# Optimization experiments

Measured on AMD Instinct MI355X. Metric: run time of the kernel, lower is better.

## Reference

```python
import jax, jax.numpy as jnp
import numpy as np

N = 4096
CIN = 128
COUT = 128
J = 2
DENSITY = 0.01  # ~40 nonzeros per Laplacian row


def _mask(k):
    m = (jax.random.uniform(k, (N, N)) < DENSITY).astype(jnp.float32)
    # Laplacians have nonzero diagonals; also guarantees no empty softmax rows
    return jnp.maximum(m, jnp.eye(N, dtype=jnp.float32))


def setup_inputs() -> dict:
    key = jax.random.key(0)
    ks = jax.random.split(key, 9)
    x = jax.random.normal(ks[0], (N, CIN), dtype=jnp.float32)
    Lup = _mask(ks[1])
    Ldown = _mask(ks[2])
    P = jax.random.normal(ks[3], (N, N), dtype=jnp.float32) / np.float32(np.sqrt(N))
    weight_irr = jax.random.normal(ks[4], (J, CIN, COUT), dtype=jnp.float32) * 0.05
    weight_sol = jax.random.normal(ks[5], (J, CIN, COUT), dtype=jnp.float32) * 0.05
    weight_har = jax.random.normal(ks[6], (CIN, COUT), dtype=jnp.float32) * 0.05
    att_irr = jax.random.normal(ks[7], (2 * J * COUT, 1), dtype=jnp.float32) * 0.05
    att_sol = jax.random.normal(ks[8], (2 * J * COUT, 1), dtype=jnp.float32) * 0.05
    return {"x": x, "Lup": Lup, "Ldown": Ldown, "P": P,
            "weight_irr": weight_irr, "weight_sol": weight_sol,
            "weight_har": weight_har, "att_irr": att_irr, "att_sol": att_sol}


def _masked_row_softmax(e, mask):
    # torch.sparse.softmax over the mask's nonzero pattern, dim=1, then to_dense
    on = mask > 0
    z = jnp.where(on, e, -jnp.inf)
    m = jnp.max(z, axis=1, keepdims=True)
    m = jnp.where(jnp.isfinite(m), m, 0.0)  # guard fully-masked rows
    p = jnp.exp(z - m)                      # exp(-inf)=0 off-pattern
    s = jnp.sum(p, axis=1, keepdims=True)
    s = jnp.where(s == 0, 1.0, s)
    return jnp.where(on, p / s, 0.0)


def _branch(x, weight, att, mask):
    j, cout = weight.shape[0], weight.shape[2]
    att_slice = j * cout
    h = jnp.einsum('ni,jio->jno', x, weight)         # [J, N, Cout]
    hf = h.reshape(-1, att_slice)                    # [N, J*Cout] (row-major, as torch)
    src = hf @ att[:att_slice]                       # [N, 1]
    dst = hf @ att[att_slice:]                       # [N, 1]
    e = jax.nn.leaky_relu(src + dst.T)               # [N, N], slope 0.01 (torch default)
    alpha = _masked_row_softmax(e, mask)             # [N, N]
    powers = [alpha]
    for _ in range(j - 1):
        powers.append(powers[-1] @ alpha)            # iterative matrix powers
    alpha_exp = jnp.stack(powers)                    # [J, N, N]
    # torch.sum with no dim: full reduction to a SCALAR (faithful to source)
    return jnp.sum(jnp.einsum('jnm,jmo->jno', alpha_exp, h))


def reference(x, Lup, Ldown, P, weight_irr, weight_sol, weight_har, att_irr, att_sol):
    z_irr = _branch(x, weight_irr, att_irr, Ldown)   # scalar
    z_sol = _branch(x, weight_sol, att_sol, Lup)     # scalar
    z_har = (P @ x) @ weight_har                     # [N, Cout]
    return z_irr + z_sol + z_har
```

## Files before the change

### kernel.cpp

```cpp
#include <hip/hip_runtime.h>

typedef __attribute__((ext_vector_type(8))) short short8b;
typedef __attribute__((ext_vector_type(4))) float f32x4;

#define NEG_SENTINEL (-1e30f)

constexpr int C_OFF    = 0;
constexpr int C2_OFF   = 8192;
constexpr int SC_OFF   = 16384;
constexpr int FLAG_I   = 16390;
constexpr int ZERO_N   = 16448;
constexpr int V_OFF    = 16448;
constexpr int NP_OFF   = 19008;
constexpr int SRC_OFF  = 100928;
constexpr int RM_OFF   = 117312;
constexpr int RS_OFF   = 125504;
constexpr int NNZ_OFF  = 133696;
constexpr int CCI_OFF  = 141888;
constexpr int XBT_OFF  = 666176;
constexpr int TP_OFF   = 928320;

__device__ __forceinline__ unsigned short f2bf(float f) {
  unsigned int u = __float_as_uint(f);
  u += 0x7FFFu + ((u >> 16) & 1u);
  return (unsigned short)(u >> 16);
}
__device__ __forceinline__ float bf2f(unsigned short b) {
  return __uint_as_float(((unsigned int)b) << 16);
}
__device__ __forceinline__ float scrub(float v) {
  unsigned int u = __float_as_uint(v);
  return ((u & 0x7F800000u) == 0x7F800000u) ? 0.f : v;
}

__global__ __launch_bounds__(128) void k_vvec(const void* __restrict__ xin,
                                              const void* __restrict__ w_irr,
                                              const void* __restrict__ w_sol,
                                              const void* __restrict__ att_irr,
                                              const void* __restrict__ att_sol,
                                              int* __restrict__ flagp,
                                              float* __restrict__ vvec) {
  __shared__ int sdet[128];
  int t = threadIdx.x;
  unsigned int ef = (((const unsigned int*)xin)[t] >> 7) & 0xFFu;
  sdet[t] = (ef >= 100u && ef <= 150u) ? 1 : 0;
  __syncthreads();
  for (int d = 64; d > 0; d >>= 1) { if (t < d) sdet[t] += sdet[t + d]; __syncthreads(); }
  int f = (sdet[0] >= 96) ? 1 : 0;
  if (blockIdx.x == 0 && t == 0) *flagp = f;
  int bx = blockIdx.x;
  int b = bx / 10, rem = bx % 10, j = rem / 5, tt = rem % 5;
  const void* Wv = (b == 0 ? w_irr : w_sol);
  const void* Av = (b == 0 ? att_irr : att_sol);
  int i = t;
  float s = 0.f;
  if (f) {
    const unsigned short* Wr = (const unsigned short*)Wv + (size_t)j * 16384 + (size_t)i * 128;
    const unsigned short* Ar = (const unsigned short*)Av + tt * 128;
    for (int o = 0; o < 128; o += 8) {
      uint4 wq = *(const uint4*)(Wr + o);
      unsigned int ww[4] = {wq.x, wq.y, wq.z, wq.w};
      float cf[8];
      if (tt < 4) {
        uint4 aq = *(const uint4*)(Ar + o);
        unsigned int aa[4] = {aq.x, aq.y, aq.z, aq.w};
#pragma unroll
        for (int u = 0; u < 4; ++u) {
          cf[2 * u] = bf2f((unsigned short)(aa[u] & 0xFFFFu));
          cf[2 * u + 1] = bf2f((unsigned short)(aa[u] >> 16));
        }
      } else {
#pragma unroll
        for (int e = 0; e < 8; ++e) cf[e] = 1.0f;
      }
#pragma unroll
      for (int u = 0; u < 4; ++u) {
        s += bf2f((unsigned short)(ww[u] & 0xFFFFu)) * cf[2 * u];
        s += bf2f((unsigned short)(ww[u] >> 16)) * cf[2 * u + 1];
      }
    }
  } else {
    const float* Wr = (const float*)Wv + (size_t)j * 16384 + (size_t)i * 128;
    const float* Ar = (const float*)Av + tt * 128;
    for (int o = 0; o < 128; o += 4) {
      float4 wq = *(const float4*)(Wr + o);
      float4 aq = {1.f, 1.f, 1.f, 1.f};
      if (tt < 4) aq = *(const float4*)(Ar + o);
      s += wq.x * aq.x + wq.y * aq.y + wq.z * aq.z + wq.w * aq.w;
    }
  }
  vvec[bx * 128 + i] = s;
}

__global__ __launch_bounds__(256) void k_prep(const void* __restrict__ xin,
                                              const int* __restrict__ flag,
                                              const float* __restrict__ vvec,
                                              unsigned short* __restrict__ xbT,
                                              float* __restrict__ np,
                                              float* __restrict__ srcdst) {
  __shared__ __align__(16) float ldsx[64 * 130];
  __shared__ __align__(16) float ldsv[2560];
  __shared__ float ldsp[4 * 1280];
  __shared__ float npl[1280];
  int f = *flag;
  int t = threadIdx.x, nb = blockIdx.x * 64;
  for (int q = 0; q < 16; ++q) {
    int idx = q * 256 + t;
    int row = idx >> 6, cp = idx & 63;
    float vx, vy;
    if (f) {
      unsigned int u = ((const unsigned int*)xin)[(size_t)(nb + row) * 64 + cp];
      vx = bf2f((unsigned short)(u & 0xFFFFu));
      vy = bf2f((unsigned short)(u >> 16));
    } else {
      float2 v = ((const float2*)xin)[(size_t)(nb + row) * 64 + cp];
      vx = v.x; vy = v.y;
    }
    ldsx[row * 130 + cp * 2] = vx;
    ldsx[row * 130 + cp * 2 + 1] = vy;
  }
  for (int q = 0; q < 10; ++q) { int idx = q * 256 + t; ldsv[idx] = vvec[idx]; }
  __syncthreads();
  for (int q = 0; q < 32; ++q) {
    int idx = q * 256 + t;
    int c = idx >> 6, n = idx & 63;
    xbT[(size_t)c * 4096 + nb + n] = f2bf(ldsx[n * 130 + c]);
  }
  int row = t & 63, qq = t >> 6, i0 = qq * 32;
  float acc[20];
#pragma unroll
  for (int k = 0; k < 20; ++k) acc[k] = 0.f;
  for (int i = i0; i < i0 + 32; i += 2) {
    float2 xv = *(const float2*)&ldsx[row * 130 + i];
#pragma unroll
    for (int k = 0; k < 20; ++k) {
      float2 vk = *(const float2*)&ldsv[k * 128 + i];
      acc[k] += xv.x * vk.x + xv.y * vk.y;
    }
  }
#pragma unroll
  for (int k = 0; k < 20; ++k) ldsp[qq * 1280 + row * 20 + k] = acc[k];
  __syncthreads();
  for (int rep = 0; rep < 5; ++rep) {
    int idx = rep * 256 + t;
    int k = idx >> 6, rr = idx & 63;
    float s = ldsp[rr * 20 + k] + ldsp[1280 + rr * 20 + k] +
              ldsp[2560 + rr * 20 + k] + ldsp[3840 + rr * 20 + k];
    npl[k * 64 + rr] = s;
    np[(size_t)k * 4096 + nb + rr] = s;
  }
  __syncthreads();
  {
    int b = t >> 7, j = (t >> 6) & 1, kind = (t >> 5) & 1, q = t & 31;
    int bl = q * 2;
    int r = j * 2048 + (nb >> 1) + q;
    int kidx = b * 10 + j * 5 + kind * 2;
    float val = npl[kidx * 64 + bl] + npl[(kidx + 1) * 64 + bl + 1];
    srcdst[b * 8192 + kind * 4096 + r] = val;
  }
}

__device__ __forceinline__ int col_of(int f, int l, int bit) {
  if (f) return ((bit >> 3) * 512) + l * 8 + (bit & 7);
  return ((bit >> 5) * 2048) + (((bit >> 2) & 7) * 256) + l * 4 + (bit & 3);
}

__global__ __launch_bounds__(256) void k_scan(const void* __restrict__ Ldown,
                                              const void* __restrict__ Lup,
                                              float* __restrict__ ws) {
  int b = blockIdx.y, t = threadIdx.x;
  int wid = t >> 6, l = t & 63;
  int r = blockIdx.x * 4 + wid;
  int f = ((const int*)ws)[FLAG_I];
  unsigned short* cci = (unsigned short*)(ws + CCI_OFF) + (size_t)(b * 4096 + r) * 128;
  unsigned long long hm = 0ULL;
  if (f) {
    const uint4* rp = (const uint4*)((const unsigned short*)(b ? Lup : Ldown) +
                                     (size_t)r * 4096) + l;
    uint4 cs[8];
#pragma unroll
    for (int it = 0; it < 8; ++it) cs[it] = rp[it * 64];
#pragma unroll
    for (int it = 0; it < 8; ++it) {
      unsigned int wv[4] = {cs[it].x, cs[it].y, cs[it].z, cs[it].w};
#pragma unroll
      for (int u = 0; u < 4; ++u) {
        hm |= ((unsigned long long)((wv[u] & 0xFFFFu) != 0u)) << (it * 8 + u * 2);
        hm |= ((unsigned long long)((wv[u] >> 16) != 0u)) << (it * 8 + u * 2 + 1);
      }
    }
  } else {
    const uint4* rp = (const uint4*)((const float*)(b ? Lup : Ldown) +
                                     (size_t)r * 4096) + l;
#pragma unroll
    for (int p = 0; p < 2; ++p) {
      uint4 cs[8];
#pragma unroll
      for (int it = 0; it < 8; ++it) cs[it] = rp[(p * 8 + it) * 64];
#pragma unroll
      for (int it = 0; it < 8; ++it) {
        unsigned int wv[4] = {cs[it].x, cs[it].y, cs[it].z, cs[it].w};
#pragma unroll
        for (int u = 0; u < 4; ++u)
          hm |= ((unsigned long long)(wv[u] != 0u)) << (p * 32 + it * 4 + u);
      }
    }
  }
  int cnt = __popcll(hm);
  int pre = cnt;
  for (int d = 1; d < 64; d <<= 1) {
    int o = __shfl_up(pre, d);
    if (l >= d) pre += o;
  }
  int base = pre - cnt;
  int nz = __shfl(pre, 63);
  if (l == 0) ((int*)ws)[NNZ_OFF + b * 4096 + r] = min(nz, 128);
  const float* srcp = ws + SRC_OFF + b * 8192;
  const float* dstp = srcp + 4096;
  float srcr = srcp[r];
  float mx = NEG_SENTINEL, sm = 0.f;
  unsigned long long mm = hm;
  while (mm) {
    int bit = __builtin_ctzll(mm); mm &= mm - 1;
    int m = col_of(f, l, bit);
    float e = srcr + dstp[m];
    e = (e >= 0.f) ? e : 0.01f * e;
    if (e > mx) { sm = sm * __expf(mx - e) + 1.f; mx = e; }
    else        { sm += __expf(e - mx); }
  }
  for (int d = 1; d < 64; d <<= 1) {
    float om = __shfl_xor(mx, d);
    float os = __shfl_xor(sm, d);
    float M = fmaxf(mx, om);
    sm = sm * __expf(mx - M) + os * __expf(om - M);
    mx = M;
  }
  if (l == 0) {
    ws[RM_OFF + b * 4096 + r] = mx;
    ws[RS_OFF + b * 4096 + r] = sm;
  }
  float inv = 1.0f / sm;
  int slot = base;
  mm = hm;
  while (mm) {
    int bit = __builtin_ctzll(mm); mm &= mm - 1;
    int m = col_of(f, l, bit);
    if (slot < 128) cci[slot] = (unsigned short)m;
    ++slot;
    float e = srcr + dstp[m];
    e = (e >= 0.f) ? e : 0.01f * e;
    atomicAdd(&ws[C_OFF + b * 4096 + m], __expf(e - mx) * inv);
  }
}

__device__ __forceinline__ float alpha_of(const float* ws, int b, int r, int m) {
  const float* srcp = ws + SRC_OFF + b * 8192;
  float e = srcp[r] + srcp[4096 + m];
  e = (e >= 0.f) ? e : 0.01f * e;
  return __expf(e - ws[RM_OFF + b * 4096 + r]) / ws[RS_OFF + b * 4096 + r];
}

__global__ __launch_bounds__(256) void k_c2(float* __restrict__ ws) {
  int b = blockIdx.y;
  int s = blockIdx.x * 256 + threadIdx.x;
  int r = s >> 7, k = s & 127;
  int nz = ((const int*)ws)[NNZ_OFF + b * 4096 + r];
  if (k < nz) {
    int m = ((const unsigned short*)(ws + CCI_OFF))[(size_t)(b * 4096 + r) * 128 + k];
    atomicAdd(&ws[C2_OFF + b * 4096 + m], ws[C_OFF + b * 4096 + r] * alpha_of(ws, b, r, m));
  }
}

__global__ __launch_bounds__(256) void k_scalar(float* __restrict__ ws) {
  int b = blockIdx.x, t = threadIdx.x;
  const float* cb  = ws + C_OFF  + b * 4096;
  const float* c2b = ws + C2_OFF + b * 4096;
  const float* hr0 = ws + NP_OFF + (b * 10 + 4) * 4096;
  const float* hr1 = ws + NP_OFF + (b * 10 + 9) * 4096;
  double acc = 0.0;
  for (int m = t; m < 4096; m += 256)
    acc += (double)scrub(cb[m]) * (double)scrub(hr0[m]) +
           (double)scrub(c2b[m]) * (double)scrub(hr1[m]);
  __shared__ double sd[256];
  sd[t] = acc;
  __syncthreads();
  for (int s = 128; s > 0; s >>= 1) { if (t < s) sd[t] += sd[t + s]; __syncthreads(); }
  if (t == 0) atomicAdd(&ws[SC_OFF], (float)sd[0]);
}

__global__ __launch_bounds__(256) void k_gemm1(const void* __restrict__ P,
                                               const unsigned short* __restrict__ xbT,
                                               const int* __restrict__ flag,
                                               float* __restrict__ TP) {
  __shared__ __align__(16) unsigned short a_lds[64 * 40];
  __shared__ __align__(16) unsigned short b_lds[128 * 40];
  int f = *flag;
  const int mt = blockIdx.x & 63, ks = blockIdx.x >> 6;
  const int mb = mt * 64;
  const int t = threadIdx.x;
  const int w = t >> 6, l = t & 63, quad = l >> 4, lr = l & 15;
  f32x4 acc[8] = {};
  const int arow = t >> 2, akq = (t & 3) << 3;
  const int bn = t >> 1, bh = (t & 1) << 4;
  const int k0 = ks * 512;
  uint4 aU, bU0, bU1;
#define LOADT(IT)                                                              \
  {                                                                            \
    const int kb = k0 + (IT) * 32;                                             \
    if (f) {                                                                   \
      aU = *(const uint4*)((const unsigned short*)P +                          \
                           (size_t)(mb + arow) * 4096 + kb + akq);             \
    } else {                                                                   \
      const float* pa = (const float*)P + (size_t)(mb + arow) * 4096 + kb + akq; \
      float4 f0 = *(const float4*)pa;                                          \
      float4 f1 = *(const float4*)(pa + 4);                                    \
      unsigned short u[8] = {f2bf(f0.x), f2bf(f0.y), f2bf(f0.z), f2bf(f0.w),   \
                             f2bf(f1.x), f2bf(f1.y), f2bf(f1.z), f2bf(f1.w)};  \
      aU = *(const uint4*)u;                                                   \
    }                                                                          \
    const unsigned short* src = xbT + (size_t)bn * 4096 + kb + bh;             \
    bU0 = *(const uint4*)src;                                                  \
    bU1 = *(const uint4*)(src + 8);                                            \
  }
  LOADT(0);
  for (int it = 0; it < 16; ++it) {
    *(uint4*)&a_lds[arow * 40 + akq] = aU;
    *(uint4*)&b_lds[bn * 40 + bh] = bU0;
    *(uint4*)&b_lds[bn * 40 + bh + 8] = bU1;
    __syncthreads();
    if (it < 15) LOADT(it + 1);
    short8b af = *(short8b*)&a_lds[(w * 16 + lr) * 40 + quad * 8];
#pragma unroll
    for (int nt = 0; nt < 8; ++nt) {
      short8b bf = *(short8b*)&b_lds[(nt * 16 + lr) * 40 + quad * 8];
      acc[nt] = __builtin_amdgcn_mfma_f32_16x16x32_bf16(af, bf, acc[nt], 0, 0, 0);
    }
    if (it < 15) __syncthreads();
  }
#undef LOADT
  float* Tp = TP + (size_t)ks * 524288;
#pragma unroll
  for (int nt = 0; nt < 8; ++nt)
#pragma unroll
    for (int rr = 0; rr < 4; ++rr) {
      int row = mb + w * 16 + quad * 4 + rr;
      int col = nt * 16 + lr;
      Tp[(size_t)row * 128 + col] = acc[nt][rr];
    }
}

__global__ __launch_bounds__(256) void k_gemm2(const float* __restrict__ TP,
                                               const void* __restrict__ W,
                                               const float* __restrict__ ws,
                                               void* __restrict__ outv) {
  __shared__ float tl[16 * 128];
  int f = ((const int*)ws)[FLAG_I];
  int t = threadIdx.x;
  int rb = blockIdx.x * 16;
  for (int q = 0; q < 2; ++q) {
    int vi = q * 256 + t;
    size_t base = (size_t)rb * 128 + (size_t)vi * 4;
    float4 s = {0.f, 0.f, 0.f, 0.f};
#pragma unroll
    for (int p = 0; p < 8; ++p) {
      float4 v = *(const float4*)&TP[(size_t)p * 524288 + base];
      s.x += v.x; s.y += v.y; s.z += v.z; s.w += v.w;
    }
    *(float4*)&tl[vi * 4] = s;
  }
  __syncthreads();
  int col = t & 127, rg = t >> 7;
  int r0 = rg * 8;
  float acc[8] = {};
  for (int k = 0; k < 128; k += 4) {
    float w0, w1, w2, w3;
    if (f) {
      const unsigned short* W16 = (const unsigned short*)W;
      w0 = bf2f(W16[(k + 0) * 128 + col]); w1 = bf2f(W16[(k + 1) * 128 + col]);
      w2 = bf2f(W16[(k + 2) * 128 + col]); w3 = bf2f(W16[(k + 3) * 128 + col]);
    } else {
      const float* W32 = (const float*)W;
      w0 = W32[(k + 0) * 128 + col]; w1 = W32[(k + 1) * 128 + col];
      w2 = W32[(k + 2) * 128 + col]; w3 = W32[(k + 3) * 128 + col];
    }
#pragma unroll
    for (int rr = 0; rr < 8; ++rr) {
      float4 tv = *(const float4*)&tl[(r0 + rr) * 128 + k];
      acc[rr] += tv.x * w0 + tv.y * w1 + tv.z * w2 + tv.w * w3;
    }
  }
  float s = scrub(ws[SC_OFF]);
#pragma unroll
  for (int rr = 0; rr < 8; ++rr) {
    size_t oi = (size_t)(rb + r0 + rr) * 128 + col;
    float v = s + acc[rr];
    if (f) ((unsigned short*)outv)[oi] = f2bf(v);
    else   ((float*)outv)[oi] = v;
  }
}

extern "C" void kernel_launch(void* const* d_in, const int* in_sizes, int n_in,
                              void* d_out, int out_size, void* d_ws, size_t ws_size,
                              hipStream_t stream) {
  const void* x       = d_in[0];
  const void* Lup     = d_in[1];
  const void* Ldown   = d_in[2];
  const void* P       = d_in[3];
  const void* w_irr   = d_in[4];
  const void* w_sol   = d_in[5];
  const void* w_har   = d_in[6];
  const void* att_irr = d_in[7];
  const void* att_sol = d_in[8];
  float* ws = (float*)d_ws;

  hipMemsetAsync(d_ws, 0, (size_t)ZERO_N * sizeof(float), stream);
  k_vvec  <<<20, 128, 0, stream>>>(x, w_irr, w_sol, att_irr, att_sol,
                                   (int*)ws + FLAG_I, ws + V_OFF);
  k_prep  <<<64, 256, 0, stream>>>(x, (int*)ws + FLAG_I, ws + V_OFF,
                                   (unsigned short*)(ws + XBT_OFF), ws + NP_OFF,
                                   ws + SRC_OFF);
  k_gemm1 <<<512, 256, 0, stream>>>(P, (const unsigned short*)(ws + XBT_OFF),
                                    (int*)ws + FLAG_I, ws + TP_OFF);
  k_scan  <<<dim3(1024, 2), 256, 0, stream>>>(Ldown, Lup, ws);
  k_c2    <<<dim3(2048, 2), 256, 0, stream>>>(ws);
  k_scalar<<<2, 256, 0, stream>>>(ws);
  k_gemm2 <<<256, 256, 0, stream>>>(ws + TP_OFF, w_har, ws, d_out);
}
```

Baseline: 308.1 us.

## Split softmax into a separate kernel with cached alpha values, and reorder launches

The mask-scan kernel now only compacts column indices. A new k_smax kernel computes the row softmax from the compacted indices with one wave per row and two values per lane, stores the alpha values, and scatters them into C. k_c2 reads the stored alpha values instead of recomputing exp and divide per nonzero, and its grid is halved to one wave per row. The sparse kernels now launch before gemm1 because the alpha buffer aliases the TP region that gemm1 writes. This adds a kernel launch and an extra buffer round trip in exchange for less divergent serial work in the scan.

```diff
diff --git a/kernel.cpp b/kernel.cpp
--- a/kernel.cpp
+++ b/kernel.cpp
@@ -19,6 +19,7 @@
 constexpr int CCI_OFF  = 141888;
 constexpr int XBT_OFF  = 666176;
 constexpr int TP_OFF   = 928320;
+constexpr int AV_OFF   = 928320;
 
 __device__ __forceinline__ unsigned short f2bf(float f) {
   unsigned int u = __float_as_uint(f);
@@ -215,60 +216,71 @@
   int base = pre - cnt;
   int nz = __shfl(pre, 63);
   if (l == 0) ((int*)ws)[NNZ_OFF + b * 4096 + r] = min(nz, 128);
-  const float* srcp = ws + SRC_OFF + b * 8192;
-  const float* dstp = srcp + 4096;
-  float srcr = srcp[r];
-  float mx = NEG_SENTINEL, sm = 0.f;
+  int slot = base;
   unsigned long long mm = hm;
-  while (mm) {
-    int bit = __builtin_ctzll(mm); mm &= mm - 1;
-    int m = col_of(f, l, bit);
-    float e = srcr + dstp[m];
-    e = (e >= 0.f) ? e : 0.01f * e;
-    if (e > mx) { sm = sm * __expf(mx - e) + 1.f; mx = e; }
-    else        { sm += __expf(e - mx); }
-  }
-  for (int d = 1; d < 64; d <<= 1) {
-    float om = __shfl_xor(mx, d);
-    float os = __shfl_xor(sm, d);
-    float M = fmaxf(mx, om);
-    sm = sm * __expf(mx - M) + os * __expf(om - M);
-    mx = M;
-  }
-  if (l == 0) {
-    ws[RM_OFF + b * 4096 + r] = mx;
-    ws[RS_OFF + b * 4096 + r] = sm;
-  }
-  float inv = 1.0f / sm;
-  int slot = base;
-  mm = hm;
   while (mm) {
     int bit = __builtin_ctzll(mm); mm &= mm - 1;
     int m = col_of(f, l, bit);
     if (slot < 128) cci[slot] = (unsigned short)m;
     ++slot;
-    float e = srcr + dstp[m];
-    e = (e >= 0.f) ? e : 0.01f * e;
-    atomicAdd(&ws[C_OFF + b * 4096 + m], __expf(e - mx) * inv);
-  }
-}
-
-__device__ __forceinline__ float alpha_of(const float* ws, int b, int r, int m) {
+  }
+}
+
+__global__ __launch_bounds__(256) void k_smax(float* __restrict__ ws) {
+  int b = blockIdx.y, t = threadIdx.x;
+  int wid = t >> 6, l = t & 63;
+  int r = blockIdx.x * 4 + wid;
+  int nz = ((const int*)ws)[NNZ_OFF + b * 4096 + r];
+  const unsigned short* cci =
+      (const unsigned short*)(ws + CCI_OFF) + (size_t)(b * 4096 + r) * 128;
   const float* srcp = ws + SRC_OFF + b * 8192;
-  float e = srcp[r] + srcp[4096 + m];
-  e = (e >= 0.f) ? e : 0.01f * e;
-  return __expf(e - ws[RM_OFF + b * 4096 + r]) / ws[RS_OFF + b * 4096 + r];
+  const float* dstp = srcp + 4096;
+  float srcr = srcp[r];
+  int m0 = 0, m1 = 0;
+  float e0 = NEG_SENTINEL, e1 = NEG_SENTINEL;
+  if (l < nz) {
+    m0 = cci[l];
+    float e = srcr + dstp[m0];
+    e0 = (e >= 0.f) ? e : 0.01f * e;
+  }
+  if (l + 64 < nz) {
+    m1 = cci[l + 64];
+    float e = srcr + dstp[m1];
+    e1 = (e >= 0.f) ? e : 0.01f * e;
+  }
+  float mx = fmaxf(e0, e1);
+  for (int d = 1; d < 64; d <<= 1) mx = fmaxf(mx, __shfl_xor(mx, d));
+  float p0 = (l < nz) ? __expf(e0 - mx) : 0.f;
+  float p1 = (l + 64 < nz) ? __expf(e1 - mx) : 0.f;
+  float sm = p0 + p1;
+  for (int d = 1; d < 64; d <<= 1) sm += __shfl_xor(sm, d);
+  float inv = 1.0f / sm;
+  float* av = ws + AV_OFF + (size_t)(b * 4096 + r) * 128;
+  if (l < nz) {
+    float a = p0 * inv;
+    av[l] = a;
+    atomicAdd(&ws[C_OFF + b * 4096 + m0], a);
+  }
+  if (l + 64 < nz) {
+    float a = p1 * inv;
+    av[l + 64] = a;
+    atomicAdd(&ws[C2_OFF - C2_OFF + C_OFF + b * 4096 + m1], a);
+  }
 }
 
 __global__ __launch_bounds__(256) void k_c2(float* __restrict__ ws) {
-  int b = blockIdx.y;
-  int s = blockIdx.x * 256 + threadIdx.x;
-  int r = s >> 7, k = s & 127;
+  int b = blockIdx.y, t = threadIdx.x;
+  int wid = t >> 6, l = t & 63;
+  int r = blockIdx.x * 4 + wid;
   int nz = ((const int*)ws)[NNZ_OFF + b * 4096 + r];
-  if (k < nz) {
-    int m = ((const unsigned short*)(ws + CCI_OFF))[(size_t)(b * 4096 + r) * 128 + k];
-    atomicAdd(&ws[C2_OFF + b * 4096 + m], ws[C_OFF + b * 4096 + r] * alpha_of(ws, b, r, m));
-  }
+  float cr = ws[C_OFF + b * 4096 + r];
+  const unsigned short* cci =
+      (const unsigned short*)(ws + CCI_OFF) + (size_t)(b * 4096 + r) * 128;
+  const float* av = ws + AV_OFF + (size_t)(b * 4096 + r) * 128;
+  if (l < nz)
+    atomicAdd(&ws[C2_OFF + b * 4096 + cci[l]], cr * av[l]);
+  if (l + 64 < nz)
+    atomicAdd(&ws[C2_OFF + b * 4096 + cci[l + 64]], cr * av[l + 64]);
 }
 
 __global__ __launch_bounds__(256) void k_scalar(float* __restrict__ ws) {
@@ -419,10 +431,11 @@
   k_prep  <<<64, 256, 0, stream>>>(x, (int*)ws + FLAG_I, ws + V_OFF,
                                    (unsigned short*)(ws + XBT_OFF), ws + NP_OFF,
                                    ws + SRC_OFF);
+  k_scan  <<<dim3(1024, 2), 256, 0, stream>>>(Ldown, Lup, ws);
+  k_smax  <<<dim3(1024, 2), 256, 0, stream>>>(ws);
+  k_c2    <<<dim3(1024, 2), 256, 0, stream>>>(ws);
+  k_scalar<<<2, 256, 0, stream>>>(ws);
   k_gemm1 <<<512, 256, 0, stream>>>(P, (const unsigned short*)(ws + XBT_OFF),
                                     (int*)ws + FLAG_I, ws + TP_OFF);
-  k_scan  <<<dim3(1024, 2), 256, 0, stream>>>(Ldown, Lup, ws);
-  k_c2    <<<dim3(2048, 2), 256, 0, stream>>>(ws);
-  k_scalar<<<2, 256, 0, stream>>>(ws);
   k_gemm2 <<<256, 256, 0, stream>>>(ws + TP_OFF, w_har, ws, d_out);
 }
```

Measured after the change: 324.9 us. 5.4% more time.

## Cache softmax alpha values in scan and stage mask rows via LDS

Applied to the files above, without the earlier changes.

k_scan now stores each computed attention probability alongside its column index, so k_c2 reads cached alpha values instead of recomputing exp and reloading the row max and sum. k_c2 is restructured to one wave per row with two entries per lane. In the bf16 mask path, rows are loaded directly into LDS with global_load_lds. Because the alpha cache reuses the TP region, gemm1 is moved after scan, c2 and scalar. This adds extra stores in scan and ties buffer reuse to launch order.

```diff
diff --git a/kernel.cpp b/kernel.cpp
--- a/kernel.cpp
+++ b/kernel.cpp
@@ -4,6 +4,8 @@
 typedef __attribute__((ext_vector_type(4))) float f32x4;
 
 #define NEG_SENTINEL (-1e30f)
+#define GLOBAL_AS __attribute__((address_space(1)))
+#define LDS_AS __attribute__((address_space(3)))
 
 constexpr int C_OFF    = 0;
 constexpr int C2_OFF   = 8192;
@@ -19,6 +21,7 @@
 constexpr int CCI_OFF  = 141888;
 constexpr int XBT_OFF  = 666176;
 constexpr int TP_OFF   = 928320;
+constexpr int AV_OFF   = 928320;
 
 __device__ __forceinline__ unsigned short f2bf(float f) {
   unsigned int u = __float_as_uint(f);
@@ -168,6 +171,7 @@
 __global__ __launch_bounds__(256) void k_scan(const void* __restrict__ Ldown,
                                               const void* __restrict__ Lup,
                                               float* __restrict__ ws) {
+  __shared__ __align__(16) unsigned short rows[4][4096];
   int b = blockIdx.y, t = threadIdx.x;
   int wid = t >> 6, l = t & 63;
   int r = blockIdx.x * 4 + wid;
@@ -175,14 +179,21 @@
   unsigned short* cci = (unsigned short*)(ws + CCI_OFF) + (size_t)(b * 4096 + r) * 128;
   unsigned long long hm = 0ULL;
   if (f) {
-    const uint4* rp = (const uint4*)((const unsigned short*)(b ? Lup : Ldown) +
-                                     (size_t)r * 4096) + l;
-    uint4 cs[8];
-#pragma unroll
-    for (int it = 0; it < 8; ++it) cs[it] = rp[it * 64];
+    const unsigned short* gsrc = (const unsigned short*)(b ? Lup : Ldown) +
+                                 (size_t)r * 4096 + l * 8;
+    unsigned short* ldst = &rows[wid][0];
+#pragma unroll
+    for (int j = 0; j < 8; ++j) {
+      __builtin_amdgcn_global_load_lds(
+          (const GLOBAL_AS unsigned int*)(gsrc + j * 512),
+          (LDS_AS unsigned int*)(ldst + j * 512), 16, 0, 0);
+    }
+    asm volatile("s_waitcnt vmcnt(0)" ::: "memory");
+    __builtin_amdgcn_sched_barrier(0);
 #pragma unroll
     for (int it = 0; it < 8; ++it) {
-      unsigned int wv[4] = {cs[it].x, cs[it].y, cs[it].z, cs[it].w};
+      uint4 cs = *(const uint4*)&rows[wid][it * 512 + l * 8];
+      unsigned int wv[4] = {cs.x, cs.y, cs.z, cs.w};
 #pragma unroll
       for (int u = 0; u < 4; ++u) {
         hm |= ((unsigned long long)((wv[u] & 0xFFFFu) != 0u)) << (it * 8 + u * 2);
@@ -235,40 +246,39 @@
     sm = sm * __expf(mx - M) + os * __expf(om - M);
     mx = M;
   }
-  if (l == 0) {
-    ws[RM_OFF + b * 4096 + r] = mx;
-    ws[RS_OFF + b * 4096 + r] = sm;
-  }
   float inv = 1.0f / sm;
+  float* av = ws + AV_OFF + (size_t)(b * 4096 + r) * 128;
   int slot = base;
   mm = hm;
   while (mm) {
     int bit = __builtin_ctzll(mm); mm &= mm - 1;
     int m = col_of(f, l, bit);
-    if (slot < 128) cci[slot] = (unsigned short)m;
-    ++slot;
     float e = srcr + dstp[m];
     e = (e >= 0.f) ? e : 0.01f * e;
-    atomicAdd(&ws[C_OFF + b * 4096 + m], __expf(e - mx) * inv);
-  }
-}
-
-__device__ __forceinline__ float alpha_of(const float* ws, int b, int r, int m) {
-  const float* srcp = ws + SRC_OFF + b * 8192;
-  float e = srcp[r] + srcp[4096 + m];
-  e = (e >= 0.f) ? e : 0.01f * e;
-  return __expf(e - ws[RM_OFF + b * 4096 + r]) / ws[RS_OFF + b * 4096 + r];
+    float p = __expf(e - mx) * inv;
+    if (slot < 128) { cci[slot] = (unsigned short)m; av[slot] = p; }
+    ++slot;
+    atomicAdd(&ws[C_OFF + b * 4096 + m], p);
+  }
 }
 
 __global__ __launch_bounds__(256) void k_c2(float* __restrict__ ws) {
-  int b = blockIdx.y;
-  int s = blockIdx.x * 256 + threadIdx.x;
-  int r = s >> 7, k = s & 127;
+  int b = blockIdx.y, t = threadIdx.x;
+  int wid = t >> 6, l = t & 63;
+  int r = blockIdx.x * 4 + wid;
+  const unsigned short* cci =
+      (const unsigned short*)(ws + CCI_OFF) + (size_t)(b * 4096 + r) * 128;
+  const float* av = ws + AV_OFF + (size_t)(b * 4096 + r) * 128;
+  int m0 = cci[l];
+  int m1 = cci[l + 64];
+  float a0 = av[l];
+  float a1 = av[l + 64];
+  float cr = ws[C_OFF + b * 4096 + r];
   int nz = ((const int*)ws)[NNZ_OFF + b * 4096 + r];
-  if (k < nz) {
-    int m = ((const unsigned short*)(ws + CCI_OFF))[(size_t)(b * 4096 + r) * 128 + k];
-    atomicAdd(&ws[C2_OFF + b * 4096 + m], ws[C_OFF + b * 4096 + r] * alpha_of(ws, b, r, m));
-  }
+  if (l < nz)
+    atomicAdd(&ws[C2_OFF + b * 4096 + m0], cr * a0);
+  if (l + 64 < nz)
+    atomicAdd(&ws[C2_OFF + b * 4096 + m1], cr * a1);
 }
 
 __global__ __launch_bounds__(256) void k_scalar(float* __restrict__ ws) {
@@ -419,10 +429,10 @@
   k_prep  <<<64, 256, 0, stream>>>(x, (int*)ws + FLAG_I, ws + V_OFF,
                                    (unsigned short*)(ws + XBT_OFF), ws + NP_OFF,
                                    ws + SRC_OFF);
+  k_scan  <<<dim3(1024, 2), 256, 0, stream>>>(Ldown, Lup, ws);
+  k_c2    <<<dim3(1024, 2), 256, 0, stream>>>(ws);
+  k_scalar<<<2, 256, 0, stream>>>(ws);
   k_gemm1 <<<512, 256, 0, stream>>>(P, (const unsigned short*)(ws + XBT_OFF),
                                     (int*)ws + FLAG_I, ws + TP_OFF);
-  k_scan  <<<dim3(1024, 2), 256, 0, stream>>>(Ldown, Lup, ws);
-  k_c2    <<<dim3(2048, 2), 256, 0, stream>>>(ws);
-  k_scalar<<<2, 256, 0, stream>>>(ws);
   k_gemm2 <<<256, 256, 0, stream>>>(ws + TP_OFF, w_har, ws, d_out);
 }
```

Result: no change. 312.7 us (+1.5%).

## Fuse kernels: merge vvec into prep, gemm1+scan into one grid, replace c2/scalar

Applied to the files above, without the earlier changes.

Folds the workspace memset and the attention-vector reduction into the prep kernel. The P@x GEMM and the sparse mask scan now run as one launch of 2560 blocks, so the two independent workloads can overlap on the GPU. The second-power atomic scatter (k_c2) and the scalar reduction are replaced by a per-row gather kernel that computes alpha^2·h as c·(alpha·h1), avoiding the second atomic buffer. This cuts launch count and atomics, at the cost of a heterogeneous uber-kernel and float rather than double accumulation in the final sum.

```diff
diff --git a/kernel.cpp b/kernel.cpp
--- a/kernel.cpp
+++ b/kernel.cpp
@@ -6,11 +6,9 @@
 #define NEG_SENTINEL (-1e30f)
 
 constexpr int C_OFF    = 0;
-constexpr int C2_OFF   = 8192;
 constexpr int SC_OFF   = 16384;
 constexpr int FLAG_I   = 16390;
 constexpr int ZERO_N   = 16448;
-constexpr int V_OFF    = 16448;
 constexpr int NP_OFF   = 19008;
 constexpr int SRC_OFF  = 100928;
 constexpr int RM_OFF   = 117312;
@@ -33,68 +31,12 @@
   return ((u & 0x7F800000u) == 0x7F800000u) ? 0.f : v;
 }
 
-__global__ __launch_bounds__(128) void k_vvec(const void* __restrict__ xin,
+__global__ __launch_bounds__(256) void k_prep(const void* __restrict__ xin,
                                               const void* __restrict__ w_irr,
                                               const void* __restrict__ w_sol,
                                               const void* __restrict__ att_irr,
                                               const void* __restrict__ att_sol,
-                                              int* __restrict__ flagp,
-                                              float* __restrict__ vvec) {
-  __shared__ int sdet[128];
-  int t = threadIdx.x;
-  unsigned int ef = (((const unsigned int*)xin)[t] >> 7) & 0xFFu;
-  sdet[t] = (ef >= 100u && ef <= 150u) ? 1 : 0;
-  __syncthreads();
-  for (int d = 64; d > 0; d >>= 1) { if (t < d) sdet[t] += sdet[t + d]; __syncthreads(); }
-  int f = (sdet[0] >= 96) ? 1 : 0;
-  if (blockIdx.x == 0 && t == 0) *flagp = f;
-  int bx = blockIdx.x;
-  int b = bx / 10, rem = bx % 10, j = rem / 5, tt = rem % 5;
-  const void* Wv = (b == 0 ? w_irr : w_sol);
-  const void* Av = (b == 0 ? att_irr : att_sol);
-  int i = t;
-  float s = 0.f;
-  if (f) {
-    const unsigned short* Wr = (const unsigned short*)Wv + (size_t)j * 16384 + (size_t)i * 128;
-    const unsigned short* Ar = (const unsigned short*)Av + tt * 128;
-    for (int o = 0; o < 128; o += 8) {
-      uint4 wq = *(const uint4*)(Wr + o);
-      unsigned int ww[4] = {wq.x, wq.y, wq.z, wq.w};
-      float cf[8];
-      if (tt < 4) {
-        uint4 aq = *(const uint4*)(Ar + o);
-        unsigned int aa[4] = {aq.x, aq.y, aq.z, aq.w};
-#pragma unroll
-        for (int u = 0; u < 4; ++u) {
-          cf[2 * u] = bf2f((unsigned short)(aa[u] & 0xFFFFu));
-          cf[2 * u + 1] = bf2f((unsigned short)(aa[u] >> 16));
-        }
-      } else {
-#pragma unroll
-        for (int e = 0; e < 8; ++e) cf[e] = 1.0f;
-      }
-#pragma unroll
-      for (int u = 0; u < 4; ++u) {
-        s += bf2f((unsigned short)(ww[u] & 0xFFFFu)) * cf[2 * u];
-        s += bf2f((unsigned short)(ww[u] >> 16)) * cf[2 * u + 1];
-      }
-    }
-  } else {
-    const float* Wr = (const float*)Wv + (size_t)j * 16384 + (size_t)i * 128;
-    const float* Ar = (const float*)Av + tt * 128;
-    for (int o = 0; o < 128; o += 4) {
-      float4 wq = *(const float4*)(Wr + o);
-      float4 aq = {1.f, 1.f, 1.f, 1.f};
-      if (tt < 4) aq = *(const float4*)(Ar + o);
-      s += wq.x * aq.x + wq.y * aq.y + wq.z * aq.z + wq.w * aq.w;
-    }
-  }
-  vvec[bx * 128 + i] = s;
-}
-
-__global__ __launch_bounds__(256) void k_prep(const void* __restrict__ xin,
-                                              const int* __restrict__ flag,
-                                              const float* __restrict__ vvec,
+                                              float* __restrict__ ws,
                                               unsigned short* __restrict__ xbT,
                                               float* __restrict__ np,
                                               float* __restrict__ srcdst) {
@@ -102,8 +44,67 @@
   __shared__ __align__(16) float ldsv[2560];
   __shared__ float ldsp[4 * 1280];
   __shared__ float npl[1280];
-  int f = *flag;
+  __shared__ int sdet[128];
   int t = threadIdx.x, nb = blockIdx.x * 64;
+  for (int i = blockIdx.x * 256 + t; i < ZERO_N; i += 16384) ws[i] = 0.f;
+  if (t < 128) {
+    unsigned int ef = (((const unsigned int*)xin)[t] >> 7) & 0xFFu;
+    sdet[t] = (ef >= 100u && ef <= 150u) ? 1 : 0;
+  }
+  __syncthreads();
+  for (int d = 64; d > 0; d >>= 1) { if (t < d) sdet[t] += sdet[t + d]; __syncthreads(); }
+  int f = (sdet[0] >= 96) ? 1 : 0;
+  if (blockIdx.x == 0 && t == 0) ((int*)ws)[FLAG_I] = f;
+  for (int p = t; p < 512; p += 256) {
+    int b = p >> 8, j = (p >> 7) & 1, i = p & 127;
+    const void* Wv = (b == 0 ? w_irr : w_sol);
+    const void* Av = (b == 0 ? att_irr : att_sol);
+    float sv[4] = {0.f, 0.f, 0.f, 0.f};
+    float s4 = 0.f;
+    if (f) {
+      const unsigned short* Wr = (const unsigned short*)Wv + (size_t)j * 16384 + (size_t)i * 128;
+      const unsigned short* Ar = (const unsigned short*)Av;
+      for (int o = 0; o < 128; o += 8) {
+        uint4 wq = *(const uint4*)(Wr + o);
+        unsigned int ww[4] = {wq.x, wq.y, wq.z, wq.w};
+        float wf[8];
+#pragma unroll
+        for (int u = 0; u < 4; ++u) {
+          wf[2 * u] = bf2f((unsigned short)(ww[u] & 0xFFFFu));
+          wf[2 * u + 1] = bf2f((unsigned short)(ww[u] >> 16));
+          s4 += wf[2 * u] + wf[2 * u + 1];
+        }
+#pragma unroll
+        for (int tt = 0; tt < 4; ++tt) {
+          uint4 aq = *(const uint4*)(Ar + tt * 128 + o);
+          unsigned int aa[4] = {aq.x, aq.y, aq.z, aq.w};
+#pragma unroll
+          for (int u = 0; u < 4; ++u) {
+            sv[tt] += wf[2 * u] * bf2f((unsigned short)(aa[u] & 0xFFFFu));
+            sv[tt] += wf[2 * u + 1] * bf2f((unsigned short)(aa[u] >> 16));
+          }
+        }
+      }
+    } else {
+      const float* Wr = (const float*)Wv + (size_t)j * 16384 + (size_t)i * 128;
+      const float* Ar = (const float*)Av;
+      for (int o = 0; o < 128; o += 4) {
+        float4 wq = *(const float4*)(Wr + o);
+        s4 += wq.x + wq.y + wq.z + wq.w;
+#pragma unroll
+        for (int tt = 0; tt < 4; ++tt) {
+          float4 aq = *(const float4*)(Ar + tt * 128 + o);
+          sv[tt] += wq.x * aq.x + wq.y * aq.y + wq.z * aq.z + wq.w * aq.w;
+        }
+      }
+    }
+    int kb = (b * 10 + j * 5) * 128 + i;
+    ldsv[kb] = sv[0];
+    ldsv[kb + 128] = sv[1];
+    ldsv[kb + 256] = sv[2];
+    ldsv[kb + 384] = sv[3];
+    ldsv[kb + 512] = s4;
+  }
   for (int q = 0; q < 16; ++q) {
     int idx = q * 256 + t;
     int row = idx >> 6, cp = idx & 63;
@@ -119,7 +120,6 @@
     ldsx[row * 130 + cp * 2] = vx;
     ldsx[row * 130 + cp * 2 + 1] = vy;
   }
-  for (int q = 0; q < 10; ++q) { int idx = q * 256 + t; ldsv[idx] = vvec[idx]; }
   __syncthreads();
   for (int q = 0; q < 32; ++q) {
     int idx = q * 256 + t;
@@ -147,7 +147,7 @@
     float s = ldsp[rr * 20 + k] + ldsp[1280 + rr * 20 + k] +
               ldsp[2560 + rr * 20 + k] + ldsp[3840 + rr * 20 + k];
     npl[k * 64 + rr] = s;
-    np[(size_t)k * 4096 + nb + rr] = s;
+    if ((k % 5) == 4) np[(size_t)k * 4096 + nb + rr] = s;
   }
   __syncthreads();
   {
@@ -165,145 +165,25 @@
   return ((bit >> 5) * 2048) + (((bit >> 2) & 7) * 256) + l * 4 + (bit & 3);
 }
 
-__global__ __launch_bounds__(256) void k_scan(const void* __restrict__ Ldown,
+__global__ __launch_bounds__(256) void k_uber(const void* __restrict__ P,
+                                              const void* __restrict__ Ldown,
                                               const void* __restrict__ Lup,
-                                              float* __restrict__ ws) {
-  int b = blockIdx.y, t = threadIdx.x;
-  int wid = t >> 6, l = t & 63;
-  int r = blockIdx.x * 4 + wid;
-  int f = ((const int*)ws)[FLAG_I];
-  unsigned short* cci = (unsigned short*)(ws + CCI_OFF) + (size_t)(b * 4096 + r) * 128;
-  unsigned long long hm = 0ULL;
-  if (f) {
-    const uint4* rp = (const uint4*)((const unsigned short*)(b ? Lup : Ldown) +
-                                     (size_t)r * 4096) + l;
-    uint4 cs[8];
-#pragma unroll
-    for (int it = 0; it < 8; ++it) cs[it] = rp[it * 64];
-#pragma unroll
-    for (int it = 0; it < 8; ++it) {
-      unsigned int wv[4] = {cs[it].x, cs[it].y, cs[it].z, cs[it].w};
-#pragma unroll
-      for (int u = 0; u < 4; ++u) {
-        hm |= ((unsigned long long)((wv[u] & 0xFFFFu) != 0u)) << (it * 8 + u * 2);
-        hm |= ((unsigned long long)((wv[u] >> 16) != 0u)) << (it * 8 + u * 2 + 1);
-      }
-    }
-  } else {
-    const uint4* rp = (const uint4*)((const float*)(b ? Lup : Ldown) +
-                                     (size_t)r * 4096) + l;
-#pragma unroll
-    for (int p = 0; p < 2; ++p) {
-      uint4 cs[8];
-#pragma unroll
-      for (int it = 0; it < 8; ++it) cs[it] = rp[(p * 8 + it) * 64];
-#pragma unroll
-      for (int it = 0; it < 8; ++it) {
-        unsigned int wv[4] = {cs[it].x, cs[it].y, cs[it].z, cs[it].w};
-#pragma unroll
-        for (int u = 0; u < 4; ++u)
-          hm |= ((unsigned long long)(wv[u] != 0u)) << (p * 32 + it * 4 + u);
-      }
-    }
-  }
-  int cnt = __popcll(hm);
-  int pre = cnt;
-  for (int d = 1; d < 64; d <<= 1) {
-    int o = __shfl_up(pre, d);
-    if (l >= d) pre += o;
-  }
-  int base = pre - cnt;
-  int nz = __shfl(pre, 63);
-  if (l == 0) ((int*)ws)[NNZ_OFF + b * 4096 + r] = min(nz, 128);
-  const float* srcp = ws + SRC_OFF + b * 8192;
-  const float* dstp = srcp + 4096;
-  float srcr = srcp[r];
-  float mx = NEG_SENTINEL, sm = 0.f;
-  unsigned long long mm = hm;
-  while (mm) {
-    int bit = __builtin_ctzll(mm); mm &= mm - 1;
-    int m = col_of(f, l, bit);
-    float e = srcr + dstp[m];
-    e = (e >= 0.f) ? e : 0.01f * e;
-    if (e > mx) { sm = sm * __expf(mx - e) + 1.f; mx = e; }
-    else        { sm += __expf(e - mx); }
-  }
-  for (int d = 1; d < 64; d <<= 1) {
-    float om = __shfl_xor(mx, d);
-    float os = __shfl_xor(sm, d);
-    float M = fmaxf(mx, om);
-    sm = sm * __expf(mx - M) + os * __expf(om - M);
-    mx = M;
-  }
-  if (l == 0) {
-    ws[RM_OFF + b * 4096 + r] = mx;
-    ws[RS_OFF + b * 4096 + r] = sm;
-  }
-  float inv = 1.0f / sm;
-  int slot = base;
-  mm = hm;
-  while (mm) {
-    int bit = __builtin_ctzll(mm); mm &= mm - 1;
-    int m = col_of(f, l, bit);
-    if (slot < 128) cci[slot] = (unsigned short)m;
-    ++slot;
-    float e = srcr + dstp[m];
-    e = (e >= 0.f) ? e : 0.01f * e;
-    atomicAdd(&ws[C_OFF + b * 4096 + m], __expf(e - mx) * inv);
-  }
-}
-
-__device__ __forceinline__ float alpha_of(const float* ws, int b, int r, int m) {
-  const float* srcp = ws + SRC_OFF + b * 8192;
-  float e = srcp[r] + srcp[4096 + m];
-  e = (e >= 0.f) ? e : 0.01f * e;
-  return __expf(e - ws[RM_OFF + b * 4096 + r]) / ws[RS_OFF + b * 4096 + r];
-}
-
-__global__ __launch_bounds__(256) void k_c2(float* __restrict__ ws) {
-  int b = blockIdx.y;
-  int s = blockIdx.x * 256 + threadIdx.x;
-  int r = s >> 7, k = s & 127;
-  int nz = ((const int*)ws)[NNZ_OFF + b * 4096 + r];
-  if (k < nz) {
-    int m = ((const unsigned short*)(ws + CCI_OFF))[(size_t)(b * 4096 + r) * 128 + k];
-    atomicAdd(&ws[C2_OFF + b * 4096 + m], ws[C_OFF + b * 4096 + r] * alpha_of(ws, b, r, m));
-  }
-}
-
-__global__ __launch_bounds__(256) void k_scalar(float* __restrict__ ws) {
-  int b = blockIdx.x, t = threadIdx.x;
-  const float* cb  = ws + C_OFF  + b * 4096;
-  const float* c2b = ws + C2_OFF + b * 4096;
-  const float* hr0 = ws + NP_OFF + (b * 10 + 4) * 4096;
-  const float* hr1 = ws + NP_OFF + (b * 10 + 9) * 4096;
-  double acc = 0.0;
-  for (int m = t; m < 4096; m += 256)
-    acc += (double)scrub(cb[m]) * (double)scrub(hr0[m]) +
-           (double)scrub(c2b[m]) * (double)scrub(hr1[m]);
-  __shared__ double sd[256];
-  sd[t] = acc;
-  __syncthreads();
-  for (int s = 128; s > 0; s >>= 1) { if (t < s) sd[t] += sd[t + s]; __syncthreads(); }
-  if (t == 0) atomicAdd(&ws[SC_OFF], (float)sd[0]);
-}
-
-__global__ __launch_bounds__(256) void k_gemm1(const void* __restrict__ P,
-                                               const unsigned short* __restrict__ xbT,
-                                               const int* __restrict__ flag,
-                                               float* __restrict__ TP) {
+                                              const unsigned short* __restrict__ xbT,
+                                              float* __restrict__ ws,
+                                              float* __restrict__ TP) {
   __shared__ __align__(16) unsigned short a_lds[64 * 40];
   __shared__ __align__(16) unsigned short b_lds[128 * 40];
-  int f = *flag;
-  const int mt = blockIdx.x & 63, ks = blockIdx.x >> 6;
-  const int mb = mt * 64;
+  int f = ((const int*)ws)[FLAG_I];
   const int t = threadIdx.x;
-  const int w = t >> 6, l = t & 63, quad = l >> 4, lr = l & 15;
-  f32x4 acc[8] = {};
-  const int arow = t >> 2, akq = (t & 3) << 3;
-  const int bn = t >> 1, bh = (t & 1) << 4;
-  const int k0 = ks * 512;
-  uint4 aU, bU0, bU1;
+  if (blockIdx.x < 512) {
+    const int mt = blockIdx.x & 63, ks = blockIdx.x >> 6;
+    const int mb = mt * 64;
+    const int w = t >> 6, l = t & 63, quad = l >> 4, lr = l & 15;
+    f32x4 acc[8] = {};
+    const int arow = t >> 2, akq = (t & 3) << 3;
+    const int bn = t >> 1, bh = (t & 1) << 4;
+    const int k0 = ks * 512;
+    uint4 aU, bU0, bU1;
 #define LOADT(IT)                                                              \
   {                                                                            \
     const int kb = k0 + (IT) * 32;                                             \
@@ -322,31 +202,150 @@
     bU0 = *(const uint4*)src;                                                  \
     bU1 = *(const uint4*)(src + 8);                                            \
   }
-  LOADT(0);
-  for (int it = 0; it < 16; ++it) {
-    *(uint4*)&a_lds[arow * 40 + akq] = aU;
-    *(uint4*)&b_lds[bn * 40 + bh] = bU0;
-    *(uint4*)&b_lds[bn * 40 + bh + 8] = bU1;
-    __syncthreads();
-    if (it < 15) LOADT(it + 1);
-    short8b af = *(short8b*)&a_lds[(w * 16 + lr) * 40 + quad * 8];
-#pragma unroll
-    for (int nt = 0; nt < 8; ++nt) {
-      short8b bf = *(short8b*)&b_lds[(nt * 16 + lr) * 40 + quad * 8];
-      acc[nt] = __builtin_amdgcn_mfma_f32_16x16x32_bf16(af, bf, acc[nt], 0, 0, 0);
-    }
-    if (it < 15) __syncthreads();
-  }
+    LOADT(0);
+    for (int it = 0; it < 16; ++it) {
+      *(uint4*)&a_lds[arow * 40 + akq] = aU;
+      *(uint4*)&b_lds[bn * 40 + bh] = bU0;
+      *(uint4*)&b_lds[bn * 40 + bh + 8] = bU1;
+      __syncthreads();
+      if (it < 15) LOADT(it + 1);
+      short8b af = *(short8b*)&a_lds[(w * 16 + lr) * 40 + quad * 8];
+#pragma unroll
+      for (int nt = 0; nt < 8; ++nt) {
+        short8b bf = *(short8b*)&b_lds[(nt * 16 + lr) * 40 + quad * 8];
+        acc[nt] = __builtin_amdgcn_mfma_f32_16x16x32_bf16(af, bf, acc[nt], 0, 0, 0);
+      }
+      if (it < 15) __syncthreads();
+    }
 #undef LOADT
-  float* Tp = TP + (size_t)ks * 524288;
-#pragma unroll
-  for (int nt = 0; nt < 8; ++nt)
-#pragma unroll
-    for (int rr = 0; rr < 4; ++rr) {
-      int row = mb + w * 16 + quad * 4 + rr;
-      int col = nt * 16 + lr;
-      Tp[(size_t)row * 128 + col] = acc[nt][rr];
-    }
+    float* Tp = TP + (size_t)ks * 524288;
+#pragma unroll
+    for (int nt = 0; nt < 8; ++nt)
+#pragma unroll
+      for (int rr = 0; rr < 4; ++rr) {
+        int row = mb + w * 16 + quad * 4 + rr;
+        int col = nt * 16 + lr;
+        Tp[(size_t)row * 128 + col] = acc[nt][rr];
+      }
+  } else {
+    int sid = blockIdx.x - 512;
+    int b = sid >> 10, rowblk = sid & 1023;
+    int wid = t >> 6, l = t & 63;
+    int r = rowblk * 4 + wid;
+    unsigned short* cci = (unsigned short*)(ws + CCI_OFF) + (size_t)(b * 4096 + r) * 128;
+    unsigned long long hm = 0ULL;
+    if (f) {
+      const uint4* rp = (const uint4*)((const unsigned short*)(b ? Lup : Ldown) +
+                                       (size_t)r * 4096) + l;
+      uint4 cs[8];
+#pragma unroll
+      for (int it = 0; it < 8; ++it) cs[it] = rp[it * 64];
+#pragma unroll
+      for (int it = 0; it < 8; ++it) {
+        unsigned int wv[4] = {cs[it].x, cs[it].y, cs[it].z, cs[it].w};
+#pragma unroll
+        for (int u = 0; u < 4; ++u) {
+          hm |= ((unsigned long long)((wv[u] & 0xFFFFu) != 0u)) << (it * 8 + u * 2);
+          hm |= ((unsigned long long)((wv[u] >> 16) != 0u)) << (it * 8 + u * 2 + 1);
+        }
+      }
+    } else {
+      const uint4* rp = (const uint4*)((const float*)(b ? Lup : Ldown) +
+                                       (size_t)r * 4096) + l;
+#pragma unroll
+      for (int p = 0; p < 2; ++p) {
+        uint4 cs[8];
+#pragma unroll
+        for (int it = 0; it < 8; ++it) cs[it] = rp[(p * 8 + it) * 64];
+#pragma unroll
+        for (int it = 0; it < 8; ++it) {
+          unsigned int wv[4] = {cs[it].x, cs[it].y, cs[it].z, cs[it].w};
+#pragma unroll
+          for (int u = 0; u < 4; ++u)
+            hm |= ((unsigned long long)(wv[u] != 0u)) << (p * 32 + it * 4 + u);
+        }
+      }
+    }
+    int cnt = __popcll(hm);
+    int pre = cnt;
+    for (int d = 1; d < 64; d <<= 1) {
+      int o = __shfl_up(pre, d);
+      if (l >= d) pre += o;
+    }
+    int base = pre - cnt;
+    int nz = __shfl(pre, 63);
+    if (l == 0) ((int*)ws)[NNZ_OFF + b * 4096 + r] = min(nz, 128);
+    const float* srcp = ws + SRC_OFF + b * 8192;
+    const float* dstp = srcp + 4096;
+    float srcr = srcp[r];
+    float mx = NEG_SENTINEL, sm = 0.f;
+    unsigned long long mm = hm;
+    while (mm) {
+      int bit = __builtin_ctzll(mm); mm &= mm - 1;
+      int m = col_of(f, l, bit);
+      float e = srcr + dstp[m];
+      e = (e >= 0.f) ? e : 0.01f * e;
+      if (e > mx) { sm = sm * __expf(mx - e) + 1.f; mx = e; }
+      else        { sm += __expf(e - mx); }
+    }
+    for (int d = 1; d < 64; d <<= 1) {
+      float om = __shfl_xor(mx, d);
+      float os = __shfl_xor(sm, d);
+      float M = fmaxf(mx, om);
+      sm = sm * __expf(mx - M) + os * __expf(om - M);
+      mx = M;
+    }
+    if (l == 0) {
+      ws[RM_OFF + b * 4096 + r] = mx;
+      ws[RS_OFF + b * 4096 + r] = sm;
+    }
+    float inv = 1.0f / sm;
+    int slot = base;
+    mm = hm;
+    while (mm) {
+      int bit = __builtin_ctzll(mm); mm &= mm - 1;
+      int m = col_of(f, l, bit);
+      if (slot < 128) cci[slot] = (unsigned short)m;
+      ++slot;
+      float e = srcr + dstp[m];
+      e = (e >= 0.f) ? e : 0.01f * e;
+      atomicAdd(&ws[C_OFF + b * 4096 + m], __expf(e - mx) * inv);
+    }
+  }
+}
+
+__global__ __launch_bounds__(256) void k_fin(float* __restrict__ ws) {
+  int b = blockIdx.y, t = threadIdx.x;
+  int wid = t >> 6, l = t & 63;
+  int r = blockIdx.x * 4 + wid;
+  int nz = ((const int*)ws)[NNZ_OFF + b * 4096 + r];
+  const unsigned short* cci =
+      (const unsigned short*)(ws + CCI_OFF) + (size_t)(b * 4096 + r) * 128;
+  const float* srcp = ws + SRC_OFF + b * 8192;
+  const float* dstp = srcp + 4096;
+  const float* hr1 = ws + NP_OFF + (size_t)(b * 10 + 9) * 4096;
+  const float* hr0 = ws + NP_OFF + (size_t)(b * 10 + 4) * 4096;
+  float srcr = srcp[r];
+  float rm = ws[RM_OFF + b * 4096 + r];
+  float inv = 1.0f / ws[RS_OFF + b * 4096 + r];
+  float cr = scrub(ws[C_OFF + b * 4096 + r]);
+  int m0 = cci[l];
+  int m1 = cci[l + 64];
+  float part = 0.f;
+  if (l < nz) {
+    float e = srcr + dstp[m0];
+    e = (e >= 0.f) ? e : 0.01f * e;
+    part += __expf(e - rm) * inv * scrub(hr1[m0]);
+  }
+  if (l + 64 < nz) {
+    float e = srcr + dstp[m1];
+    e = (e >= 0.f) ? e : 0.01f * e;
+    part += __expf(e - rm) * inv * scrub(hr1[m1]);
+  }
+  part *= cr;
+  if (l == 0) part += cr * scrub(hr0[r]);
+  for (int d = 1; d < 64; d <<= 1) part += __shfl_xor(part, d);
+  if (l == 0) atomicAdd(&ws[SC_OFF], part);
 }
 
 __global__ __launch_bounds__(256) void k_gemm2(const float* __restrict__ TP,
@@ -413,16 +412,12 @@
   const void* att_sol = d_in[8];
   float* ws = (float*)d_ws;
 
-  hipMemsetAsync(d_ws, 0, (size_t)ZERO_N * sizeof(float), stream);
-  k_vvec  <<<20, 128, 0, stream>>>(x, w_irr, w_sol, att_irr, att_sol,
-                                   (int*)ws + FLAG_I, ws + V_OFF);
-  k_prep  <<<64, 256, 0, stream>>>(x, (int*)ws + FLAG_I, ws + V_OFF,
-                                   (unsigned short*)(ws + XBT_OFF), ws + NP_OFF,
-                                   ws + SRC_OFF);
-  k_gemm1 <<<512, 256, 0, stream>>>(P, (const unsigned short*)(ws + XBT_OFF),
-                                    (int*)ws + FLAG_I, ws + TP_OFF);
-  k_scan  <<<dim3(1024, 2), 256, 0, stream>>>(Ldown, Lup, ws);
-  k_c2    <<<dim3(2048, 2), 256, 0, stream>>>(ws);
-  k_scalar<<<2, 256, 0, stream>>>(ws);
-  k_gemm2 <<<256, 256, 0, stream>>>(ws + TP_OFF, w_har, ws, d_out);
-}
+  k_prep <<<64, 256, 0, stream>>>(x, w_irr, w_sol, att_irr, att_sol, ws,
+                                  (unsigned short*)(ws + XBT_OFF), ws + NP_OFF,
+                                  ws + SRC_OFF);
+  k_uber <<<2560, 256, 0, stream>>>(P, Ldown, Lup,
+                                    (const unsigned short*)(ws + XBT_OFF), ws,
+                                    ws + TP_OFF);
+  k_fin  <<<dim3(1024, 2), 256, 0, stream>>>(ws);
+  k_gemm2<<<256, 256, 0, stream>>>(ws + TP_OFF, w_har, ws, d_out);
+}
```

Result: slower. 372.8 us (+21.0%).
